# Optimization experiments

Hardware: AMD Instinct MI355X
Metric: run time of the kernel (lower is better)

Reference implementation:

```python
import jax, jax.numpy as jnp
import numpy as np

NPOINT = 2048
K = 32
EPS = 1e-5  # BatchNorm eps


def setup_inputs() -> dict:
    key = jax.random.key(0)
    ks = jax.random.split(key, 5)
    B, N, C = 4, 8192, 64
    xyz = jax.random.normal(ks[0], (B, N, 3), jnp.float32)
    points = jax.random.normal(ks[1], (B, C, N), jnp.float32)
    w0 = jax.random.normal(ks[2], (64, C + 3), jnp.float32) * 0.1
    w1 = jax.random.normal(ks[3], (128, 64), jnp.float32) * 0.1
    w2 = jax.random.normal(ks[4], (256, 128), jnp.float32) * 0.1
    return dict(
        xyz=xyz, points=points,
        w0=w0, g0=jnp.ones(64, jnp.float32), b0=jnp.zeros(64, jnp.float32),
        w1=w1, g1=jnp.ones(128, jnp.float32), b1=jnp.zeros(128, jnp.float32),
        w2=w2, g2=jnp.ones(256, jnp.float32), b2=jnp.zeros(256, jnp.float32),
    )


def _fps(xyz, S):
    """Farthest point sampling. xyz: (B,N,3) -> idx (B,S) int32. Starts at point 0."""
    B, N, _ = xyz.shape

    def step(carry, _):
        dmin, far = carry  # dmin: (B,N) running min sq-dist to chosen set; far: (B,) current pick
        centroid = jnp.take_along_axis(xyz, far[:, None, None], axis=1)  # (B,1,3)
        d = jnp.sum((xyz - centroid) ** 2, axis=-1)  # (B,N)
        dmin = jnp.minimum(dmin, d)
        nxt = jnp.argmax(dmin, axis=1).astype(jnp.int32)
        return (dmin, nxt), far

    init = (jnp.full((B, N), 1e10, xyz.dtype), jnp.zeros((B,), jnp.int32))
    _, idx = jax.lax.scan(step, init, None, length=S)
    return jnp.transpose(idx)  # (B,S)


def _bn_relu(x, g, b):
    """Training-mode BatchNorm over all but the channel (last) axis + ReLU. x: (B,S,K,C)."""
    mu = jnp.mean(x, axis=(0, 1, 2), keepdims=True)
    var = jnp.mean((x - mu) ** 2, axis=(0, 1, 2), keepdims=True)
    return jax.nn.relu((x - mu) * jax.lax.rsqrt(var + EPS) * g + b)


def reference(xyz, points, w0, g0, b0, w1, g1, b1, w2, g2, b2):
    B, N, _ = xyz.shape
    S = NPOINT
    idx = _fps(xyz, S)
    new_xyz = jnp.take_along_axis(xyz, idx[:, :, None], axis=1)  # (B,S,3)
    # knn: pairwise squared distances centroids -> all points
    d2 = jnp.sum((new_xyz[:, :, None, :] - xyz[:, None, :, :]) ** 2, axis=-1)  # (B,S,N)
    _, knn_idx = jax.lax.top_k(-d2, K)  # (B,S,K), sorted ascending by distance
    gather = jax.vmap(lambda p, i: p[i])  # per-batch fancy gather
    grouped = gather(xyz, knn_idx) - new_xyz[:, :, None, :]  # (B,S,K,3) relative coords
    neigh = gather(jnp.transpose(points, (0, 2, 1)), knn_idx)  # (B,S,K,C)
    feat = jnp.concatenate([grouped, neigh], axis=-1)  # (B,S,K,3+C)
    for w, g, b in ((w0, g0, b0), (w1, g1, b1), (w2, g2, b2)):
        feat = _bn_relu(jnp.einsum('bskc,oc->bsko', feat, w), g, b)
    new_points = jnp.transpose(jnp.max(feat, axis=2), (0, 2, 1))  # (B,C_out,S)
    return new_xyz, new_points
```

## Files before the change

kernel.cpp:

```cpp
#include <hip/hip_runtime.h>

#define BB 4
#define NN 8192
#define CC 64
#define SS 2048
#define KK 32
#define MROWS (BB*SS*KK)

typedef __attribute__((ext_vector_type(8))) short bf16x8_t;
typedef __attribute__((ext_vector_type(4))) float f32x4_t;
typedef __attribute__((ext_vector_type(2))) float f32x2_t;

__device__ __forceinline__ float bf2f(unsigned short u){
  union { unsigned int i; float f; } v; v.i = ((unsigned int)u) << 16; return v.f;
}
__device__ __forceinline__ unsigned short f2bf(float f){
  union { float f; unsigned int i; } v; v.f = f;
  unsigned int u = v.i;
  unsigned int r = (u + 0x7FFFu + ((u >> 16) & 1u)) >> 16;
  return (unsigned short)r;
}
__device__ __forceinline__ float i2f(int i){ union { int i; float f; } v; v.i = i; return v.f; }
__device__ __forceinline__ int f2i(float f){ union { float f; int i; } v; v.f = f; return v.i; }

__global__ void detect_kernel(const void* pts, int* flag){
  __shared__ int cnt;
  if (threadIdx.x == 0) cnt = 0;
  __syncthreads();
  unsigned short u = ((const unsigned short*)pts)[threadIdx.x];
  int e = (u >> 7) & 0xFF;
  if (e != 0 && (e < 112 || e > 143)) atomicAdd(&cnt, 1);
  __syncthreads();
  if (threadIdx.x == 0) *flag = (cnt > 32) ? 1 : 0;
}

__device__ __forceinline__ void pack_dev(const void* src, unsigned short* dst,
    int CTS, int KSTEPS, int IN, int remap, int idx, bool isf){
  int total = CTS*KSTEPS*512;
  if (idx >= total) return;
  int f = idx >> 9, lane = (idx >> 3) & 63, j = idx & 7;
  int ct = f / KSTEPS, ks = f % KSTEPS;
  int n = ct*16 + (lane & 15);
  int k = ks*32 + (lane >> 4)*8 + j;
  int ksrc;
  if (remap){ ksrc = (k < 64) ? (k + 3) : (k < 67 ? k - 64 : -1); }
  else      { ksrc = (k < IN) ? k : -1; }
  float v = 0.f;
  if (ksrc >= 0){
    size_t si = (size_t)n*IN + ksrc;
    v = isf ? ((const float*)src)[si] : bf2f(((const unsigned short*)src)[si]);
  }
  dst[idx] = f2bf(v);
}

__global__ __launch_bounds__(256) void prep_kernel(
    const void* xyz_in, const void* pts_in,
    const void* w0_in, const void* w1_in, const void* w2_in,
    const void* g0, const void* b0, const void* g1, const void* b1,
    const void* g2, const void* b2,
    float* xyzf, unsigned short* ptsb,
    unsigned short* w0p, unsigned short* w1p, unsigned short* w2p,
    float* gbf, float* stats, const int* flag)
{
  __shared__ float tile[64][65];
  int blk = blockIdx.x, tid = threadIdx.x;
  bool isf = (*flag != 0);
  if (blk < 512){
    int b = blk >> 7, n0 = (blk & 127) * 64;
    #pragma unroll
    for (int k = 0; k < 16; k++){
      int idx = k*256 + tid; int c = idx >> 6; int ni = idx & 63;
      size_t src = ((size_t)b*CC + c)*NN + n0 + ni;
      tile[c][ni] = isf ? ((const float*)pts_in)[src] : bf2f(((const unsigned short*)pts_in)[src]);
    }
    __syncthreads();
    #pragma unroll
    for (int k = 0; k < 16; k++){
      int idx = k*256 + tid; int ni = idx >> 6; int c = idx & 63;
      ptsb[((size_t)b*NN + n0 + ni)*CC + c] = f2bf(tile[c][ni]);
    }
  } else if (blk < 896){
    int i = (blk - 512)*256 + tid;
    if (i < BB*NN*3)
      xyzf[i] = isf ? ((const float*)xyz_in)[i] : bf2f(((const unsigned short*)xyz_in)[i]);
  } else if (blk < 900){
    int i = (blk - 896)*256 + tid;
    if (i < 896){
      const void* src; int off;
      if      (i < 64)  { src = g0; off = i; }
      else if (i < 128) { src = b0; off = i - 64; }
      else if (i < 256) { src = g1; off = i - 128; }
      else if (i < 384) { src = b1; off = i - 256; }
      else if (i < 640) { src = g2; off = i - 384; }
      else              { src = b2; off = i - 640; }
      gbf[i] = isf ? ((const float*)src)[off] : bf2f(((const unsigned short*)src)[off]);
      stats[i] = 0.f;
    }
  } else if (blk < 924){
    pack_dev(w0_in, w0p, 4, 3, 67, 1, (blk-900)*256 + tid, isf);
  } else if (blk < 956){
    pack_dev(w1_in, w1p, 8, 2, 64, 0, (blk-924)*256 + tid, isf);
  } else {
    pack_dev(w2_in, w2p, 16, 4, 128, 0, (blk-956)*256 + tid, isf);
  }
}

__device__ __forceinline__ unsigned mspread(unsigned v){
  v = (v | (v << 16)) & 0x030000FFu;
  v = (v | (v <<  8)) & 0x0300F00Fu;
  v = (v | (v <<  4)) & 0x030C30C3u;
  v = (v | (v <<  2)) & 0x09249249u;
  return v;
}
__global__ __launch_bounds__(1024) void morton_sort(const float* xyzf,
    float* psx, float* psy, float* psz, int* iorig){
  int b = blockIdx.x, tid = threadIdx.x;
  const float* xb = xyzf + (size_t)b*NN*3;
  __shared__ unsigned long long keys[NN];
  __shared__ float rbb[96];
  float x[8], y[8], z[8];
  {
    const float4* p4 = (const float4*)(xb + (size_t)tid*24);
    float4 A=p4[0],B2=p4[1],C=p4[2],D=p4[3],E=p4[4],F=p4[5];
    x[0]=A.x;  y[0]=A.y;  z[0]=A.z;
    x[1]=A.w;  y[1]=B2.x; z[1]=B2.y;
    x[2]=B2.z; y[2]=B2.w; z[2]=C.x;
    x[3]=C.y;  y[3]=C.z;  z[3]=C.w;
    x[4]=D.x;  y[4]=D.y;  z[4]=D.z;
    x[5]=D.w;  y[5]=E.x;  z[5]=E.y;
    x[6]=E.z;  y[6]=E.w;  z[6]=F.x;
    x[7]=F.y;  y[7]=F.z;  z[7]=F.w;
  }
  float lx=x[0],hx=x[0],ly=y[0],hy=y[0],lz=z[0],hz=z[0];
  #pragma unroll
  for (int j = 1; j < 8; j++){
    lx=fminf(lx,x[j]); hx=fmaxf(hx,x[j]);
    ly=fminf(ly,y[j]); hy=fmaxf(hy,y[j]);
    lz=fminf(lz,z[j]); hz=fmaxf(hz,z[j]);
  }
  #pragma unroll
  for (int off = 1; off < 64; off <<= 1){
    lx=fminf(lx,__shfl_xor(lx,off)); hx=fmaxf(hx,__shfl_xor(hx,off));
    ly=fminf(ly,__shfl_xor(ly,off)); hy=fmaxf(hy,__shfl_xor(hy,off));
    lz=fminf(lz,__shfl_xor(lz,off)); hz=fmaxf(hz,__shfl_xor(hz,off));
  }
  int w = tid >> 6;
  if ((tid & 63) == 0){
    rbb[w]=lx; rbb[16+w]=hx; rbb[32+w]=ly; rbb[48+w]=hy; rbb[64+w]=lz; rbb[80+w]=hz;
  }
  __syncthreads();
  #pragma unroll
  for (int i = 0; i < 16; i++){
    lx=fminf(lx,rbb[i]); hx=fmaxf(hx,rbb[16+i]);
    ly=fminf(ly,rbb[32+i]); hy=fmaxf(hy,rbb[48+i]);
    lz=fminf(lz,rbb[64+i]); hz=fmaxf(hz,rbb[80+i]);
  }
  float sx = 1023.0f/fmaxf(hx-lx,1e-20f);
  float sy = 1023.0f/fmaxf(hy-ly,1e-20f);
  float sz = 1023.0f/fmaxf(hz-lz,1e-20f);
  #pragma unroll
  for (int j = 0; j < 8; j++){
    int qx = (int)((x[j]-lx)*sx); qx = qx < 0 ? 0 : (qx > 1023 ? 1023 : qx);
    int qy = (int)((y[j]-ly)*sy); qy = qy < 0 ? 0 : (qy > 1023 ? 1023 : qy);
    int qz = (int)((z[j]-lz)*sz); qz = qz < 0 ? 0 : (qz > 1023 ? 1023 : qz);
    unsigned code = mspread((unsigned)qx) | (mspread((unsigned)qy) << 1) | (mspread((unsigned)qz) << 2);
    keys[tid*8 + j] = (((unsigned long long)code) << 13) | (unsigned)(tid*8 + j);
  }
  __syncthreads();
  for (int size = 2; size <= NN; size <<= 1){
    for (int stride = size >> 1; stride > 0; stride >>= 1){
      #pragma unroll 4
      for (int t = tid; t < NN/2; t += 1024){
        int pos = 2*t - (t & (stride - 1));
        bool up = (pos & size) == 0;
        unsigned long long a = keys[pos], c = keys[pos + stride];
        if ((a > c) == up){ keys[pos] = c; keys[pos + stride] = a; }
      }
      __syncthreads();
    }
  }
  #pragma unroll
  for (int j = 0; j < 8; j++){
    int i = j*1024 + tid;
    int pos = (int)(keys[i] & 8191u);
    psx[b*NN + i] = xb[pos*3];
    psy[b*NN + i] = xb[pos*3 + 1];
    psz[b*NN + i] = xb[pos*3 + 2];
    iorig[b*NN + i] = pos;
  }
}

template<int C>
__device__ __forceinline__ float dpp_maxf(float v){
  int t = __builtin_amdgcn_update_dpp(0, f2i(v), C, 0xF, 0xF, true);
  return fmaxf(v, i2f(t));
}
template<int C>
__device__ __forceinline__ unsigned dpp_minu(unsigned v){
  unsigned t = (unsigned)__builtin_amdgcn_update_dpp(-1, (int)v, C, 0xF, 0xF, false);
  return v < t ? v : t;
}

__global__ __launch_bounds__(1024, 1) void fps_kernel(const float* xyzf,
    const float* psx, const float* psy, const float* psz, const int* iorig,
    int* fps_idx, void* d_out, const int* flag){
  int b = blockIdx.x, tid = threadIdx.x;
  const float* xb = xyzf + (size_t)b*NN*3;
  __shared__ float sxyz4[NN*4];
  __shared__ unsigned long long rk[3][2];
  for (int i = tid; i < NN; i += 1024){
    const float* p = xb + (size_t)i*3;
    float4 v; v.x = p[0]; v.y = p[1]; v.z = p[2]; v.w = 0.f;
    *(float4*)&sxyz4[(size_t)i*4] = v;
  }
  if (tid < 6) ((unsigned long long*)rk)[tid] = 0ull;
  f32x2_t px2[4], py2[4], pz2[4], dmin2[4];
  int io[8];
  {
    const float4* qx = (const float4*)(psx + b*NN + tid*8);
    const float4* qy = (const float4*)(psy + b*NN + tid*8);
    const float4* qz = (const float4*)(psz + b*NN + tid*8);
    float4 a, c;
    a = qx[0]; c = qx[1];
    px2[0]=(f32x2_t){a.x,a.y}; px2[1]=(f32x2_t){a.z,a.w}; px2[2]=(f32x2_t){c.x,c.y}; px2[3]=(f32x2_t){c.z,c.w};
    a = qy[0]; c = qy[1];
    py2[0]=(f32x2_t){a.x,a.y}; py2[1]=(f32x2_t){a.z,a.w}; py2[2]=(f32x2_t){c.x,c.y}; py2[3]=(f32x2_t){c.z,c.w};
    a = qz[0]; c = qz[1];
    pz2[0]=(f32x2_t){a.x,a.y}; pz2[1]=(f32x2_t){a.z,a.w}; pz2[2]=(f32x2_t){c.x,c.y}; pz2[3]=(f32x2_t){c.z,c.w};
    const int4* qi = (const int4*)(iorig + b*NN + tid*8);
    int4 i0 = qi[0], i1 = qi[1];
    io[0]=i0.x; io[1]=i0.y; io[2]=i0.z; io[3]=i0.w;
    io[4]=i1.x; io[5]=i1.y; io[6]=i1.z; io[7]=i1.w;
  }
  #pragma unroll
  for (int q = 0; q < 4; q++) dmin2[q] = (f32x2_t){1e10f, 1e10f};
  float llx, lhx, lly, lhy, llz, lhz;
  {
    llx = fminf(fminf(px2[0].x,px2[0].y), fminf(px2[1].x,px2[1].y));
    llx = fminf(llx, fminf(fminf(px2[2].x,px2[2].y), fminf(px2[3].x,px2[3].y)));
    lhx = fmaxf(fmaxf(px2[0].x,px2[0].y), fmaxf(px2[1].x,px2[1].y));
    lhx = fmaxf(lhx, fmaxf(fmaxf(px2[2].x,px2[2].y), fmaxf(px2[3].x,px2[3].y)));
    lly = fminf(fminf(py2[0].x,py2[0].y), fminf(py2[1].x,py2[1].y));
    lly = fminf(lly, fminf(fminf(py2[2].x,py2[2].y), fminf(py2[3].x,py2[3].y)));
    lhy = fmaxf(fmaxf(py2[0].x,py2[0].y), fmaxf(py2[1].x,py2[1].y));
    lhy = fmaxf(lhy, fmaxf(fmaxf(py2[2].x,py2[2].y), fmaxf(py2[3].x,py2[3].y)));
    llz = fminf(fminf(pz2[0].x,pz2[0].y), fminf(pz2[1].x,pz2[1].y));
    llz = fminf(llz, fminf(fminf(pz2[2].x,pz2[2].y), fminf(pz2[3].x,pz2[3].y)));
    lhz = fmaxf(fmaxf(pz2[0].x,pz2[0].y), fmaxf(pz2[1].x,pz2[1].y));
    lhz = fmaxf(lhz, fmaxf(fmaxf(pz2[2].x,pz2[2].y), fmaxf(pz2[3].x,pz2[3].y)));
  }
  __syncthreads();
  int far = 0;
  bool isf32 = (*flag != 0);
  float* outf = (float*)d_out; unsigned short* outh = (unsigned short*)d_out;
  int ln = tid & 63, w = tid >> 6;
  unsigned cached_lo = 0u, cached_hi = 0u;
  float lmax = 1e10f;
  int rot = 0;
  for (int s = 0; s < SS; s++){
    int rotn = rot + 1; if (rotn == 3) rotn = 0;
    float4 cf = *(const float4*)&sxyz4[(size_t)far*4];
    float cx = cf.x, cy = cf.y, cz = cf.z;
    if (tid == 0){
      fps_idx[b*SS + s] = far;
      size_t o = ((size_t)b*SS + s)*3;
      if (isf32){ outf[o]=cx; outf[o+1]=cy; outf[o+2]=cz; }
      else { outh[o]=f2bf(cx); outh[o+1]=f2bf(cy); outh[o+2]=f2bf(cz); }
    }
    if (tid == 64){ rk[rotn][0] = 0ull; rk[rotn][1] = 0ull; }
    float dxl = fmaxf(fmaxf(llx - cx, cx - lhx), 0.f);
    float dyl = fmaxf(fmaxf(lly - cy, cy - lhy), 0.f);
    float dzl = fmaxf(fmaxf(llz - cz, cz - lhz), 0.f);
    float d2l = (dxl*dxl + dyl*dyl + dzl*dzl) * 0.99999f;
    bool upd = (s == 0) || __any(d2l < lmax);
    if (upd){
      f32x2_t cx2 = (f32x2_t){cx, cx}, cy2 = (f32x2_t){cy, cy}, cz2 = (f32x2_t){cz, cz};
      bool ch = false;
      {
        #pragma clang fp contract(off)
        #pragma unroll
        for (int q = 0; q < 4; q++){
          f32x2_t dx = px2[q] - cx2, dy = py2[q] - cy2, dz = pz2[q] - cz2;
          f32x2_t t = dx*dx;
          t = t + dy*dy;
          t = t + dz*dz;
          ch = ch | (t.x < dmin2[q].x) | (t.y < dmin2[q].y);
          dmin2[q].x = fminf(dmin2[q].x, t.x);
          dmin2[q].y = fminf(dmin2[q].y, t.y);
        }
      }
      if (__any(ch)){
        float m0 = fmaxf(fmaxf(dmin2[0].x, dmin2[0].y), fmaxf(dmin2[1].x, dmin2[1].y));
        float m1 = fmaxf(fmaxf(dmin2[2].x, dmin2[2].y), fmaxf(dmin2[3].x, dmin2[3].y));
        float lm = fmaxf(m0, m1);
        lmax = lm;
        lm = dpp_maxf<0x111>(lm); lm = dpp_maxf<0x112>(lm);
        lm = dpp_maxf<0x114>(lm); lm = dpp_maxf<0x118>(lm);
        lm = dpp_maxf<0x142>(lm); lm = dpp_maxf<0x143>(lm);
        float wmax = i2f(__builtin_amdgcn_readlane(f2i(lm), 63));
        unsigned cand = 0xFFFFFFFFu;
        #pragma unroll
        for (int q = 0; q < 4; q++){
          if (dmin2[q].x == wmax){ unsigned u = (unsigned)io[2*q];   cand = u < cand ? u : cand; }
          if (dmin2[q].y == wmax){ unsigned u = (unsigned)io[2*q+1]; cand = u < cand ? u : cand; }
        }
        cand = dpp_minu<0x111>(cand); cand = dpp_minu<0x112>(cand);
        cand = dpp_minu<0x114>(cand); cand = dpp_minu<0x118>(cand);
        cand = dpp_minu<0x142>(cand); cand = dpp_minu<0x143>(cand);
        unsigned cmin = (unsigned)__builtin_amdgcn_readlane((int)cand, 63);
        cached_hi = (unsigned)f2i(wmax);
        cached_lo = ~cmin;
      }
    }
    if (ln == 63)
      atomicMax(&rk[rot][w >> 3], (((unsigned long long)cached_hi) << 32) | cached_lo);
    __syncthreads();
    unsigned long long k0 = rk[rot][0], k1 = rk[rot][1];
    unsigned long long kk = (k1 > k0) ? k1 : k0;
    far = (int)(~(unsigned)kk);
    rot = rotn;
  }
}

__global__ __launch_bounds__(256) void knn_kernel(
    const float* psx, const float* psy, const float* psz, const int* ior,
    const float* xyzf, const int* fps_idx, int* knn){
  int cg = blockIdx.x;
  int b = cg >> 11;
  int tid = threadIdx.x;
  const float* xb = xyzf + (size_t)b*NN*3;
  __shared__ unsigned hist[4096];
  __shared__ unsigned long long cand[512];
  __shared__ unsigned psum[256];
  __shared__ unsigned exbase[64];
  __shared__ float scc[3];
  __shared__ int sB, sBase, sCl, sCc;
  __shared__ unsigned long long rmin[4];
  __shared__ unsigned long long swin;

  if (tid == 0){
    int f = fps_idx[cg];
    scc[0] = xb[f*3]; scc[1] = xb[f*3+1]; scc[2] = xb[f*3+2];
    sCl = 0; sCc = 0;
  }
  #pragma unroll
  for (int i = 0; i < 16; i++) hist[tid*16 + i] = 0;
  __syncthreads();
  float cx = scc[0], cy = scc[1], cz = scc[2];

  float dv[32]; int iv[32];
  const float4* qx = (const float4*)(psx + b*NN);
  const float4* qy = (const float4*)(psy + b*NN);
  const float4* qz = (const float4*)(psz + b*NN);
  const int4*   qi = (const int4*)(ior + b*NN);
  {
    #pragma clang fp contract(off)
    #pragma unroll
    for (int k = 0; k < 8; k++){
      float4 X = qx[k*256 + tid];
      float4 Y = qy[k*256 + tid];
      float4 Z = qz[k*256 + tid];
      int4   I = qi[k*256 + tid];
      float xs_[4] = {X.x, X.y, X.z, X.w};
      float ys_[4] = {Y.x, Y.y, Y.z, Y.w};
      float zs_[4] = {Z.x, Z.y, Z.z, Z.w};
      int   is_[4] = {I.x, I.y, I.z, I.w};
      #pragma unroll
      for (int r = 0; r < 4; r++){
        float dx = cx - xs_[r], dy = cy - ys_[r], dz = cz - zs_[r];
        dv[k*4 + r] = dx*dx + dy*dy + dz*dz;
        iv[k*4 + r] = is_[r];
      }
    }
  }
  #pragma unroll
  for (int t = 0; t < 32; t++)
    atomicAdd(&hist[((unsigned)f2i(dv[t])) >> 20], 1u);
  __syncthreads();
  unsigned lsum = 0;
  #pragma unroll
  for (int i = 0; i < 16; i++) lsum += hist[tid*16 + i];
  psum[tid] = lsum;
  __syncthreads();
  if (tid < 64){
    unsigned s4 = psum[tid*4] + psum[tid*4+1] + psum[tid*4+2] + psum[tid*4+3];
    unsigned inc = s4;
    #pragma unroll
    for (int off = 1; off < 64; off <<= 1){
      unsigned o = __shfl_up(inc, off);
      if (tid >= off) inc += o;
    }
    exbase[tid] = inc - s4;
  }
  __syncthreads();
  {
    int g4 = tid >> 2;
    unsigned ex = exbase[g4];
    for (int j = g4*4; j < tid; j++) ex += psum[j];
    unsigned run = ex;
    #pragma unroll
    for (int i = 0; i < 16; i++){
      unsigned c = hist[tid*16 + i];
      if (run < 32u && run + c >= 32u){ sB = tid*16 + i; sBase = (int)run; }
      run += c;
    }
  }
  __syncthreads();
  int Bbin = sB, base = sBase;
  int out = cg << 5;
  #pragma unroll
  for (int t = 0; t < 32; t++){
    unsigned bits = (unsigned)f2i(dv[t]);
    unsigned hb = bits >> 20;
    int idx = iv[t];
    if ((int)hb < Bbin){
      int sl = atomicAdd(&sCl, 1);
      knn[out + sl] = idx;
    } else if ((int)hb == Bbin){
      int c = atomicAdd(&sCc, 1);
      if (c < 512) cand[c] = (((unsigned long long)bits) << 32) | (unsigned)idx;
    }
  }
  __syncthreads();
  int cc = sCc; if (cc > 512) cc = 512;
  int r = 32 - base;
  for (int round = 0; round < r; round++){
    unsigned long long lm = ~0ull;
    for (int i = tid; i < cc; i += 256){
      unsigned long long v = cand[i];
      if (v < lm) lm = v;
    }
    #pragma unroll
    for (int off = 1; off < 64; off <<= 1){
      unsigned long long o = __shfl_xor(lm, off);
      if (o < lm) lm = o;
    }
    if ((tid & 63) == 0) rmin[tid >> 6] = lm;
    __syncthreads();
    if (tid == 0){
      unsigned long long m = rmin[0];
      #pragma unroll
      for (int q = 1; q < 4; q++) if (rmin[q] < m) m = rmin[q];
      swin = m;
      knn[out + base + round] = (int)(unsigned)m;
    }
    __syncthreads();
    unsigned long long m = swin;
    for (int i = tid; i < cc; i += 256)
      if (cand[i] == m) cand[i] = ~0ull;
    __syncthreads();
  }
}

__device__ __forceinline__ bf16x8_t bfrag(const unsigned short* wp, int f, int lane){
  return *(const bf16x8_t*)(wp + ((size_t)f << 9) + (lane << 3));
}
__device__ __forceinline__ bf16x8_t bn_frag(bf16x8_t v, const float* a, const float* c, int kbase){
  float4 a0 = *(const float4*)(a + kbase); float4 a1 = *(const float4*)(a + kbase + 4);
  float4 c0 = *(const float4*)(c + kbase); float4 c1 = *(const float4*)(c + kbase + 4);
  float av[8] = {a0.x,a0.y,a0.z,a0.w,a1.x,a1.y,a1.z,a1.w};
  float cv[8] = {c0.x,c0.y,c0.z,c0.w,c1.x,c1.y,c1.z,c1.w};
  bf16x8_t r;
  #pragma unroll
  for (int j = 0; j < 8; j++)
    r[j] = (short)f2bf(fmaxf(bf2f((unsigned short)v[j])*av[j] + cv[j], 0.f));
  return r;
}

template<int TILES>
__global__ __launch_bounds__(256) void passA(
    const float* __restrict__ xyzf, const unsigned short* __restrict__ ptsb,
    const int* __restrict__ fpsi, const int* __restrict__ knn,
    const unsigned short* __restrict__ w0p,
    unsigned short* __restrict__ y0g, float* osum, float* osq)
{
  __shared__ unsigned short xb0[64*104];
  __shared__ unsigned short st[64*72];
  __shared__ float sacc[128];
  int tid = threadIdx.x, lane = tid & 63, w = tid >> 6;
  int l15 = lane & 15, quad = lane >> 4;
  float ssum[4], ssq[4];
  #pragma unroll
  for (int c = 0; c < 4; c++){ ssum[c] = 0.f; ssq[c] = 0.f; }
  if (tid < 128) sacc[tid] = 0.f;
  __syncthreads();

  for (int t = 0; t < TILES; t++){
    int row0 = (blockIdx.x * TILES + t) * 64;
    {
      int r = tid >> 2, p = tid & 3;
      int g = row0 + r;
      int bq = g >> 16, s = (g >> 5) & 2047;
      int n = knn[g];
      const bf16x8_t* pr = (const bf16x8_t*)(ptsb + (((size_t)bq*NN + n) << 6));
      *(bf16x8_t*)&xb0[r*104 + p*16]     = pr[p*2];
      *(bf16x8_t*)&xb0[r*104 + p*16 + 8] = pr[p*2 + 1];
      if (p == 3){
        const float* xbp = xyzf + (size_t)bq*NN*3;
        int f = fpsi[(bq << 11) + s];
        float dx = xbp[n*3]   - xbp[f*3];
        float dy = xbp[n*3+1] - xbp[f*3+1];
        float dz = xbp[n*3+2] - xbp[f*3+2];
        bf16x8_t v = {(short)f2bf(dx), (short)f2bf(dy), (short)f2bf(dz), 0,0,0,0,0};
        bf16x8_t z = {0,0,0,0,0,0,0,0};
        *(bf16x8_t*)&xb0[r*104 + 64] = v;
        *(bf16x8_t*)&xb0[r*104 + 72] = z;
        *(bf16x8_t*)&xb0[r*104 + 80] = z;
        *(bf16x8_t*)&xb0[r*104 + 88] = z;
      }
    }
    bf16x8_t a0[3];
    #pragma unroll
    for (int ks = 0; ks < 3; ks++)
      a0[ks] = *(const bf16x8_t*)&xb0[(w*16 + l15)*104 + ks*32 + quad*8];
    #pragma unroll
    for (int ct = 0; ct < 4; ct++){
      f32x4_t a = {0.f,0.f,0.f,0.f};
      #pragma unroll
      for (int ks = 0; ks < 3; ks++)
        a = __builtin_amdgcn_mfma_f32_16x16x32_bf16(a0[ks], bfrag(w0p, ct*3+ks, lane), a, 0, 0, 0);
      #pragma unroll
      for (int r = 0; r < 4; r++){
        float v = a[r]; ssum[ct] += v; ssq[ct] += v*v;
        st[(w*16 + quad*4 + r)*72 + ct*16 + l15] = f2bf(v);
      }
    }
    __syncthreads();
    #pragma unroll
    for (int p = 0; p < 2; p++){
      int idx = p*2048 + tid*8; int r = idx >> 6; int c = idx & 63;
      *(bf16x8_t*)(y0g + (size_t)row0*64 + idx) = *(const bf16x8_t*)&st[r*72 + c];
    }
    __syncthreads();
  }
  #pragma unroll
  for (int c = 0; c < 4; c++){
    ssum[c] += __shfl_xor(ssum[c], 16); ssum[c] += __shfl_xor(ssum[c], 32);
    ssq [c] += __shfl_xor(ssq [c], 16); ssq [c] += __shfl_xor(ssq [c], 32);
  }
  if (quad == 0){
    #pragma unroll
    for (int c = 0; c < 4; c++){
      atomicAdd(&sacc[c*16 + l15], ssum[c]);
      atomicAdd(&sacc[64 + c*16 + l15], ssq[c]);
    }
  }
  __syncthreads();
  if (tid < 64){
    atomicAdd(&osum[tid], sacc[tid]);
    atomicAdd(&osq [tid], sacc[64 + tid]);
  }
}

template<int TILES>
__global__ __launch_bounds__(256) void passB(
    const unsigned short* __restrict__ y0g, const unsigned short* __restrict__ w1p,
    const float* __restrict__ stats, const float* __restrict__ gbf,
    unsigned short* __restrict__ y1g, float* osum, float* osq)
{
  __shared__ unsigned short st[64*136];
  __shared__ float sacc[256];
  __shared__ __align__(16) float sbn[128];
  int tid = threadIdx.x, lane = tid & 63, w = tid >> 6;
  int l15 = lane & 15, quad = lane >> 4;
  float ssum[8], ssq[8];
  #pragma unroll
  for (int c = 0; c < 8; c++){ ssum[c] = 0.f; ssq[c] = 0.f; }
  sacc[tid] = 0.f;
  if (tid < 64){
    const float invM = 1.0f/262144.0f;
    float mu = stats[tid]*invM;
    float var = fmaxf(stats[64+tid]*invM - mu*mu, 0.f);
    float inv = 1.0f/sqrtf(var + 1e-5f);
    float av = gbf[tid]*inv;
    sbn[tid] = av; sbn[64+tid] = gbf[64+tid] - mu*av;
  }
  __syncthreads();

  for (int t = 0; t < TILES; t++){
    int row0 = (blockIdx.x * TILES + t) * 64;
    int row = row0 + w*16 + l15;
    bf16x8_t a1[2];
    #pragma unroll
    for (int ks = 0; ks < 2; ks++){
      bf16x8_t v = *(const bf16x8_t*)(y0g + (size_t)row*64 + ks*32 + quad*8);
      a1[ks] = bn_frag(v, sbn, sbn + 64, ks*32 + quad*8);
    }
    #pragma unroll
    for (int ct = 0; ct < 8; ct++){
      f32x4_t a = {0.f,0.f,0.f,0.f};
      #pragma unroll
      for (int ks = 0; ks < 2; ks++)
        a = __builtin_amdgcn_mfma_f32_16x16x32_bf16(a1[ks], bfrag(w1p, ct*2+ks, lane), a, 0, 0, 0);
      #pragma unroll
      for (int r = 0; r < 4; r++){
        float v = a[r]; ssum[ct] += v; ssq[ct] += v*v;
        st[(w*16 + quad*4 + r)*136 + ct*16 + l15] = f2bf(v);
      }
    }
    __syncthreads();
    #pragma unroll
    for (int p = 0; p < 4; p++){
      int idx = p*2048 + tid*8; int r = idx >> 7; int c = idx & 127;
      *(bf16x8_t*)(y1g + (size_t)row0*128 + idx) = *(const bf16x8_t*)&st[r*136 + c];
    }
    __syncthreads();
  }
  #pragma unroll
  for (int c = 0; c < 8; c++){
    ssum[c] += __shfl_xor(ssum[c], 16); ssum[c] += __shfl_xor(ssum[c], 32);
    ssq [c] += __shfl_xor(ssq [c], 16); ssq [c] += __shfl_xor(ssq [c], 32);
  }
  if (quad == 0){
    #pragma unroll
    for (int c = 0; c < 8; c++){
      atomicAdd(&sacc[c*16 + l15], ssum[c]);
      atomicAdd(&sacc[128 + c*16 + l15], ssq[c]);
    }
  }
  __syncthreads();
  if (tid < 128){
    atomicAdd(&osum[tid], sacc[tid]);
    atomicAdd(&osq [tid], sacc[128 + tid]);
  }
}

template<int TILES>
__global__ __launch_bounds__(256) void passC(
    const unsigned short* __restrict__ y1g, const unsigned short* __restrict__ w2p,
    const float* __restrict__ stats, const float* __restrict__ gbf,
    float* osum, float* osq)
{
  __shared__ float sacc[512];
  __shared__ __align__(16) float sbn[256];
  int tid = threadIdx.x, lane = tid & 63, w = tid >> 6;
  int l15 = lane & 15, quad = lane >> 4;
  float ssum[16], ssq[16];
  #pragma unroll
  for (int c = 0; c < 16; c++){ ssum[c] = 0.f; ssq[c] = 0.f; }
  sacc[tid] = 0.f; sacc[tid + 256] = 0.f;
  if (tid < 128){
    const float invM = 1.0f/262144.0f;
    float mu = stats[128+tid]*invM;
    float var = fmaxf(stats[256+tid]*invM - mu*mu, 0.f);
    float inv = 1.0f/sqrtf(var + 1e-5f);
    float av = gbf[128+tid]*inv;
    sbn[tid] = av; sbn[128+tid] = gbf[256+tid] - mu*av;
  }
  __syncthreads();

  for (int t = 0; t < TILES; t++){
    int row0 = (blockIdx.x * TILES + t) * 64;
    int row = row0 + w*16 + l15;
    bf16x8_t a2[4];
    #pragma unroll
    for (int ks = 0; ks < 4; ks++){
      bf16x8_t v = *(const bf16x8_t*)(y1g + (size_t)row*128 + ks*32 + quad*8);
      a2[ks] = bn_frag(v, sbn, sbn + 128, ks*32 + quad*8);
    }
    #pragma unroll
    for (int ct = 0; ct < 16; ct++){
      f32x4_t a = {0.f,0.f,0.f,0.f};
      #pragma unroll
      for (int ks = 0; ks < 4; ks++)
        a = __builtin_amdgcn_mfma_f32_16x16x32_bf16(a2[ks], bfrag(w2p, ct*4+ks, lane), a, 0, 0, 0);
      #pragma unroll
      for (int r = 0; r < 4; r++){ float v = a[r]; ssum[ct] += v; ssq[ct] += v*v; }
    }
  }
  #pragma unroll
  for (int c = 0; c < 16; c++){
    ssum[c] += __shfl_xor(ssum[c], 16); ssum[c] += __shfl_xor(ssum[c], 32);
    ssq [c] += __shfl_xor(ssq [c], 16); ssq [c] += __shfl_xor(ssq [c], 32);
  }
  if (quad == 0){
    #pragma unroll
    for (int c = 0; c < 16; c++){
      atomicAdd(&sacc[c*16 + l15], ssum[c]);
      atomicAdd(&sacc[256 + c*16 + l15], ssq[c]);
    }
  }
  __syncthreads();
  if (tid < 256){
    atomicAdd(&osum[tid], sacc[tid]);
    atomicAdd(&osq [tid], sacc[256 + tid]);
  }
}

__global__ __launch_bounds__(256) void passD(
    const unsigned short* __restrict__ y1g, const unsigned short* __restrict__ w2p,
    const float* __restrict__ stats, const float* __restrict__ gbf,
    void* d_out, const int* __restrict__ flag)
{
  __shared__ float smax[1024];
  __shared__ __align__(16) float sbn[768];
  int tid = threadIdx.x, lane = tid & 63, w = tid >> 6;
  int l15 = lane & 15, quad = lane >> 4;
  {
    const float invM = 1.0f/262144.0f;
    if (tid < 128){
      float mu = stats[128+tid]*invM;
      float var = fmaxf(stats[256+tid]*invM - mu*mu, 0.f);
      float inv = 1.0f/sqrtf(var + 1e-5f);
      float av = gbf[128+tid]*inv;
      sbn[tid] = av; sbn[128+tid] = gbf[256+tid] - mu*av;
    }
    float mu2 = stats[384+tid]*invM;
    float var2 = fmaxf(stats[640+tid]*invM - mu2*mu2, 0.f);
    float inv2 = 1.0f/sqrtf(var2 + 1e-5f);
    float av2 = gbf[384+tid]*inv2;
    sbn[256+tid] = av2; sbn[512+tid] = gbf[640+tid] - mu2*av2;
  }
  __syncthreads();
  int row0 = blockIdx.x * 64;
  int row = row0 + w*16 + l15;
  bf16x8_t a2[4];
  #pragma unroll
  for (int ks = 0; ks < 4; ks++){
    bf16x8_t v = *(const bf16x8_t*)(y1g + (size_t)row*128 + ks*32 + quad*8);
    a2[ks] = bn_frag(v, sbn, sbn + 128, ks*32 + quad*8);
  }
  #pragma unroll
  for (int ct = 0; ct < 16; ct++){
    f32x4_t a = {0.f,0.f,0.f,0.f};
    #pragma unroll
    for (int ks = 0; ks < 4; ks++)
      a = __builtin_amdgcn_mfma_f32_16x16x32_bf16(a2[ks], bfrag(w2p, ct*4+ks, lane), a, 0, 0, 0);
    int o = ct*16 + l15;
    float ga = sbn[256 + o], gc = sbn[512 + o];
    float m = fmaxf(fmaxf(a[0]*ga + gc, a[1]*ga + gc), fmaxf(a[2]*ga + gc, a[3]*ga + gc));
    m = fmaxf(m, __shfl_xor(m, 16));
    m = fmaxf(m, __shfl_xor(m, 32));
    if (quad == 0) smax[w*256 + o] = m;
  }
  __syncthreads();
  float v0 = fmaxf(fmaxf(smax[tid], smax[256 + tid]), 0.f);
  float v1 = fmaxf(fmaxf(smax[512 + tid], smax[768 + tid]), 0.f);
  int cg = blockIdx.x * 2;
  bool isf32 = (*flag != 0);
  int b0 = cg >> 11, s0 = cg & 2047;
  int b1 = (cg+1) >> 11, s1 = (cg+1) & 2047;
  size_t o0 = (size_t)BB*SS*3 + (((size_t)(b0*256 + tid)) << 11) + s0;
  size_t o1 = (size_t)BB*SS*3 + (((size_t)(b1*256 + tid)) << 11) + s1;
  if (isf32){ ((float*)d_out)[o0] = v0; ((float*)d_out)[o1] = v1; }
  else { ((unsigned short*)d_out)[o0] = f2bf(v0); ((unsigned short*)d_out)[o1] = f2bf(v1); }
}

#define OFF_FLAG   0u
#define OFF_FPS    256u
#define OFF_KNN    33024u
#define OFF_STATS  1081600u
#define OFF_XYZF   1088768u
#define OFF_GB     1481984u
#define OFF_W0P    1485568u
#define OFF_W1P    1497856u
#define OFF_W2P    1514240u
#define OFF_PTSB   1579776u
#define OFF_Y0     5774336u
#define OFF_Y1     39328768u
#define OFF_PSX    (OFF_Y1)
#define OFF_PSY    (OFF_Y1 + 131072u)
#define OFF_PSZ    (OFF_Y1 + 262144u)
#define OFF_IOR    (OFF_Y1 + 393216u)

extern "C" void kernel_launch(void* const* d_in, const int* in_sizes, int n_in,
                              void* d_out, int out_size, void* d_ws, size_t ws_size,
                              hipStream_t stream){
  char* ws = (char*)d_ws;
  int*   flag  = (int*)(ws + OFF_FLAG);
  int*   fpsi  = (int*)(ws + OFF_FPS);
  int*   knn   = (int*)(ws + OFF_KNN);
  float* stats = (float*)(ws + OFF_STATS);
  float* xyzf  = (float*)(ws + OFF_XYZF);
  float* gbf   = (float*)(ws + OFF_GB);
  unsigned short* w0p = (unsigned short*)(ws + OFF_W0P);
  unsigned short* w1p = (unsigned short*)(ws + OFF_W1P);
  unsigned short* w2p = (unsigned short*)(ws + OFF_W2P);
  unsigned short* ptsb = (unsigned short*)(ws + OFF_PTSB);
  unsigned short* y0g = (unsigned short*)(ws + OFF_Y0);
  unsigned short* y1g = (unsigned short*)(ws + OFF_Y1);
  float* psx = (float*)(ws + OFF_PSX);
  float* psy = (float*)(ws + OFF_PSY);
  float* psz = (float*)(ws + OFF_PSZ);
  int*   ior = (int*)(ws + OFF_IOR);

  detect_kernel<<<1, 256, 0, stream>>>(d_in[1], flag);
  prep_kernel<<<1084, 256, 0, stream>>>(d_in[0], d_in[1], d_in[2], d_in[5], d_in[8],
                                        d_in[3], d_in[4], d_in[6], d_in[7], d_in[9], d_in[10],
                                        xyzf, ptsb, w0p, w1p, w2p, gbf, stats, flag);

  morton_sort<<<BB, 1024, 0, stream>>>(xyzf, psx, psy, psz, ior);
  fps_kernel<<<BB, 1024, 0, stream>>>(xyzf, psx, psy, psz, ior, fpsi, d_out, flag);
  knn_kernel<<<BB*SS, 256, 0, stream>>>(psx, psy, psz, ior, xyzf, fpsi, knn);

  passA<4><<<1024, 256, 0, stream>>>(xyzf, ptsb, fpsi, knn, w0p, y0g, stats + 0, stats + 64);
  passB<4><<<1024, 256, 0, stream>>>(y0g, w1p, stats, gbf, y1g, stats + 128, stats + 256);
  passC<4><<<1024, 256, 0, stream>>>(y1g, w2p, stats, gbf, stats + 384, stats + 640);
  passD<<<4096, 256, 0, stream>>>(y1g, w2p, stats, gbf, d_out, flag);
  (void)in_sizes; (void)n_in; (void)out_size; (void)ws_size;
}
```

Baseline: 1.851 ms.

## Replace bitonic Morton sort with shared-memory counting sort on top 13 bits

The full 8192-element bitonic sort of 64-bit Morton keys in shared memory is replaced by a counting sort into 8192 buckets taken from the top 13 bits of the 30-bit code. A histogram is built with shared atomics, prefix-summed across the block, and points are scattered with atomic cursors. This drops the many barrier-separated compare-exchange passes but loses exact Morton order within a bucket and makes ordering within a bucket nondeterministic, which may slightly change how well the later FPS and kNN stages keep spatial locality.

```diff
diff --git a/kernel.cpp b/kernel.cpp
--- a/kernel.cpp
+++ b/kernel.cpp
@@ -115,9 +115,11 @@
 __global__ __launch_bounds__(1024) void morton_sort(const float* xyzf,
     float* psx, float* psy, float* psz, int* iorig){
   int b = blockIdx.x, tid = threadIdx.x;
+  int lane = tid & 63, wid = tid >> 6;
   const float* xb = xyzf + (size_t)b*NN*3;
-  __shared__ unsigned long long keys[NN];
+  __shared__ unsigned curs[NN];
   __shared__ float rbb[96];
+  __shared__ unsigned wsum[16];
   float x[8], y[8], z[8];
   {
     const float4* p4 = (const float4*)(xb + (size_t)tid*24);
@@ -144,10 +146,10 @@
     ly=fminf(ly,__shfl_xor(ly,off)); hy=fmaxf(hy,__shfl_xor(hy,off));
     lz=fminf(lz,__shfl_xor(lz,off)); hz=fmaxf(hz,__shfl_xor(hz,off));
   }
-  int w = tid >> 6;
-  if ((tid & 63) == 0){
-    rbb[w]=lx; rbb[16+w]=hx; rbb[32+w]=ly; rbb[48+w]=hy; rbb[64+w]=lz; rbb[80+w]=hz;
-  }
+  if (lane == 0){
+    rbb[wid]=lx; rbb[16+wid]=hx; rbb[32+wid]=ly; rbb[48+wid]=hy; rbb[64+wid]=lz; rbb[80+wid]=hz;
+  }
+  for (int i = tid; i < NN; i += 1024) curs[i] = 0;
   __syncthreads();
   #pragma unroll
   for (int i = 0; i < 16; i++){
@@ -158,35 +160,45 @@
   float sx = 1023.0f/fmaxf(hx-lx,1e-20f);
   float sy = 1023.0f/fmaxf(hy-ly,1e-20f);
   float sz = 1023.0f/fmaxf(hz-lz,1e-20f);
+  unsigned bkt[8];
   #pragma unroll
   for (int j = 0; j < 8; j++){
     int qx = (int)((x[j]-lx)*sx); qx = qx < 0 ? 0 : (qx > 1023 ? 1023 : qx);
     int qy = (int)((y[j]-ly)*sy); qy = qy < 0 ? 0 : (qy > 1023 ? 1023 : qy);
     int qz = (int)((z[j]-lz)*sz); qz = qz < 0 ? 0 : (qz > 1023 ? 1023 : qz);
     unsigned code = mspread((unsigned)qx) | (mspread((unsigned)qy) << 1) | (mspread((unsigned)qz) << 2);
-    keys[tid*8 + j] = (((unsigned long long)code) << 13) | (unsigned)(tid*8 + j);
-  }
-  __syncthreads();
-  for (int size = 2; size <= NN; size <<= 1){
-    for (int stride = size >> 1; stride > 0; stride >>= 1){
-      #pragma unroll 4
-      for (int t = tid; t < NN/2; t += 1024){
-        int pos = 2*t - (t & (stride - 1));
-        bool up = (pos & size) == 0;
-        unsigned long long a = keys[pos], c = keys[pos + stride];
-        if ((a > c) == up){ keys[pos] = c; keys[pos + stride] = a; }
-      }
-      __syncthreads();
-    }
-  }
+    bkt[j] = code >> 17;
+    atomicAdd(&curs[bkt[j]], 1u);
+  }
+  __syncthreads();
+  unsigned v[8]; unsigned s = 0;
+  #pragma unroll
+  for (int j = 0; j < 8; j++){ v[j] = curs[tid*8 + j]; s += v[j]; }
+  unsigned inc = s;
+  #pragma unroll
+  for (int off = 1; off < 64; off <<= 1){
+    unsigned o = __shfl_up(inc, off);
+    if (lane >= off) inc += o;
+  }
+  if (lane == 63) wsum[wid] = inc;
+  __syncthreads();
+  if (tid == 0){
+    unsigned r = 0;
+    #pragma unroll
+    for (int i = 0; i < 16; i++){ unsigned t = wsum[i]; wsum[i] = r; r += t; }
+  }
+  __syncthreads();
+  unsigned run = wsum[wid] + inc - s;
+  #pragma unroll
+  for (int j = 0; j < 8; j++){ curs[tid*8 + j] = run; run += v[j]; }
+  __syncthreads();
   #pragma unroll
   for (int j = 0; j < 8; j++){
-    int i = j*1024 + tid;
-    int pos = (int)(keys[i] & 8191u);
-    psx[b*NN + i] = xb[pos*3];
-    psy[b*NN + i] = xb[pos*3 + 1];
-    psz[b*NN + i] = xb[pos*3 + 2];
-    iorig[b*NN + i] = pos;
+    unsigned pos = atomicAdd(&curs[bkt[j]], 1u);
+    psx[b*NN + pos] = x[j];
+    psy[b*NN + pos] = y[j];
+    psz[b*NN + pos] = z[j];
+    iorig[b*NN + pos] = tid*8 + j;
   }
 }
 
```

Measured after the change: 1.806 ms. -2.4%, faster.
